# Optimization experiments

Hardware: AMD Instinct MI355X
Metric: run time of the kernel (lower is better)

Reference implementation:

```python
import jax, jax.numpy as jnp
import numpy as np

L = 64      # max source length (x_maxL)
B = 32      # batch
DIN = 512   # input_dim
D = 512     # output_dim
FFS = 512   # filter_feats_size[-1]; conv kernel = 2*D (fwz=2) => Linear(2D -> FFS)


def setup_inputs() -> dict:
    key = jax.random.key(0)
    ks = jax.random.split(key, 5)
    def w(k, shape, fan_in):
        return jax.random.normal(k, shape, jnp.float32) * (1.0 / np.sqrt(fan_in))
    return {
        "xs_h": jax.random.normal(ks[0], (L, B, DIN), jnp.float32),
        "xs_mask": jnp.ones((L, B), jnp.float32),
        "W1": w(ks[1], (D, DIN), DIN),
        "b1": jnp.zeros((D,), jnp.float32),
        "Wc": w(ks[2], (FFS, 2 * D), 2 * D),   # Conv1d weight [FFS,1,2D] squeezed
        "bc": jnp.zeros((FFS,), jnp.float32),
        "W2": w(ks[3], (D, FFS), FFS),
        "b2": jnp.zeros((D,), jnp.float32),
    }


def _cyk_table(xs_h, W1, b1, Wc, bc, W2, b2):
    Lx, Bx, _ = xs_h.shape
    Dd = W1.shape[0]
    # diagonal: table[i][i] = l_f1(xs_h[i])
    diag = xs_h @ W1.T + b1                                  # [L,B,D]
    table = jnp.zeros((Lx, Lx, Bx, Dd), xs_h.dtype)
    ii = jnp.arange(Lx)
    table = table.at[ii, ii].set(diag)
    # wavefront over span length s: all spans (j, j+s) computed together
    for s in range(1, Lx):
        n = Lx - s                    # number of spans of this length
        j = np.arange(n)              # static indices -> efficient gather
        k = np.arange(s)              # split points offset
        left = table[j[:, None], j[:, None] + k[None, :]]            # [n,s,B,D]
        right = table[j[:, None] + k[None, :] + 1, j[:, None] + s]   # [n,s,B,D]
        comb = jnp.concatenate([left, right], axis=-1)               # [n,s,B,2D]
        # Conv1d(1, FFS, kernel=2D, stride=D) on a length-2D signal == Linear(2D->FFS)
        scores = jnp.einsum('nsbd,fd->nsbf', comb, Wc) + bc          # [n,s,B,FFS]
        node = scores.max(axis=1)                                    # max over split k
        vals = node @ W2.T + b2                                      # [n,B,D]
        table = table.at[j, j + s].set(vals)
    return table


def _cyk_mask(xs_mask, Lx):
    tri = jnp.triu(jnp.ones((Lx, Lx), xs_mask.dtype))        # [L,L]
    lengths = xs_mask.sum(axis=0)                            # [B]
    col = jnp.arange(Lx)
    keep = (col[None, :, None] < lengths[None, None, :]).astype(xs_mask.dtype)
    return tri[:, :, None] * keep                            # [L,L,B]


def reference(xs_h, xs_mask, W1, b1, Wc, bc, W2, b2):
    table = _cyk_table(xs_h, W1, b1, Wc, bc, W2, b2)
    cykmask = _cyk_mask(xs_mask, xs_h.shape[0])
    return table, cykmask
```

## Files before the change

kernel.cpp:

```cpp
#include <hip/hip_runtime.h>
#include <hip/hip_fp16.h>


#define Lx 64
#define Bb 32
#define CELLSZ (Bb*512)

typedef __attribute__((ext_vector_type(8))) short short8v;
typedef __attribute__((ext_vector_type(4))) float f32x4;

__device__ __forceinline__ int tri_idx(int a, int c) {
    return a*Lx - (a*(a-1))/2 + (c - a);
}
__device__ __forceinline__ unsigned short f2bf(float x) {
    unsigned u = __float_as_uint(x);
    unsigned r = (u + 0x7FFFu + ((u >> 16) & 1u)) >> 16;
    return (unsigned short)r;
}
__device__ __forceinline__ float bf2f(unsigned short h) {
    return __uint_as_float((unsigned)h << 16);
}
__device__ __forceinline__ size_t frag_i(int r, int c) {
    return (size_t)(r >> 4)*8192 + (c >> 3)*128 + (r & 15)*8 + (c & 7);
}
__device__ __forceinline__ unsigned pk_add_f16(unsigned a, unsigned b) {
    unsigned r;
    asm("v_pk_add_f16 %0, %1, %2" : "=v"(r) : "v"(a), "v"(b));
    return r;
}
__device__ __forceinline__ unsigned pk_max_f16(unsigned a, unsigned b) {
    unsigned r;
    asm("v_pk_max_f16 %0, %1, %2" : "=v"(r) : "v"(a), "v"(b));
    return r;
}
__device__ __forceinline__ float2 h2_to_f2(unsigned u) {
    __half2 h;
    *reinterpret_cast<unsigned*>(&h) = u;
    return __half22float2(h);
}

__device__ __forceinline__ void node_epilogue(
    unsigned a0, unsigned a1, unsigned a2, unsigned a3,
    const float* __restrict__ bc, int f0, int j, int b,
    unsigned short* __restrict__ nodeH, unsigned short* __restrict__ nodeL)
{
    float4 bcA = *(const float4*)(bc + f0);
    float4 bcB = *(const float4*)(bc + f0 + 4);
    float bcv[8] = {bcA.x,bcA.y,bcA.z,bcA.w,bcB.x,bcB.y,bcB.z,bcB.w};
    unsigned am[4] = {a0,a1,a2,a3};
    unsigned uh[4], ul[4];
    #pragma unroll
    for (int e = 0; e < 4; ++e) {
        float2 x = h2_to_f2(am[e]);
        float v0 = x.x + bcv[2*e], v1 = x.y + bcv[2*e+1];
        unsigned short h0 = f2bf(v0), h1 = f2bf(v1);
        unsigned short o0 = f2bf(v0 - bf2f(h0)), o1 = f2bf(v1 - bf2f(h1));
        uh[e] = (unsigned)h0 | ((unsigned)h1 << 16);
        ul[e] = (unsigned)o0 | ((unsigned)o1 << 16);
    }
    size_t fi = (size_t)j*16384 + frag_i(b, f0);
    *(uint4*)(nodeH + fi) = make_uint4(uh[0],uh[1],uh[2],uh[3]);
    *(uint4*)(nodeL + fi) = make_uint4(ul[0],ul[1],ul[2],ul[3]);
}


__global__ void k_zero_lower(float* __restrict__ table) {
    int cell = blockIdx.x >> 4;
    int i = cell >> 6, j = cell & 63;
    if (j >= i) return;
    int sub = blockIdx.x & 15;
    f32x4* p = (f32x4*)(table + (size_t)cell*CELLSZ) + sub*256 + threadIdx.x;
    __builtin_nontemporal_store((f32x4){0.f,0.f,0.f,0.f}, p);
}

__global__ void k_lengths(const float* __restrict__ xs_mask, float* __restrict__ lengths) {
    int b = threadIdx.x;
    if (b < Bb) {
        float s = 0.f;
        for (int i = 0; i < Lx; ++i) s += xs_mask[i*Bb + b];
        lengths[b] = s;
    }
}

__global__ void k_mask(const float* __restrict__ lengths, float* __restrict__ mask_out) {
    int idx = blockIdx.x*256 + threadIdx.x;
    int b = idx & 31;
    int j = (idx >> 5) & 63;
    int i = idx >> 11;
    float v = (j >= i && (float)j < lengths[b]) ? 1.f : 0.f;
    __builtin_nontemporal_store(v, mask_out + idx);
}

__global__ void k_bias(const float* __restrict__ b2, const float* __restrict__ Wc,
                       float* __restrict__ biasBig) {
    int c = blockIdx.x*256 + threadIdx.x;
    if (c >= 1536) return;
    if (c < 512) { biasBig[c] = b2[c]; return; }
    int p = (c - 512) & 511;
    int dofs = (c < 1024) ? 0 : 512;
    float s = 0.f;
    for (int d = 0; d < 512; ++d) s += b2[d] * Wc[p*1024 + dofs + d];
    biasBig[c] = s;
}

__global__ void k_prep_xh(const float* __restrict__ xs_h,
                          unsigned short* __restrict__ xhH, unsigned short* __restrict__ xhL) {
    int gid = blockIdx.x*256 + threadIdx.x;
    int cell = gid >> 14, e = gid & 16383;
    int b = e >> 9, d = e & 511;
    float v = xs_h[gid];
    unsigned short h = f2bf(v);
    size_t fi = (size_t)cell*16384 + frag_i(b, d);
    xhH[fi] = h; xhL[fi] = f2bf(v - bf2f(h));
}

__global__ void k_prep_w1(const float* __restrict__ W1,
                          unsigned short* __restrict__ WH, unsigned short* __restrict__ WL) {
    int gid = blockIdx.x*256 + threadIdx.x;
    int c = gid >> 9, k = gid & 511;
    float v = W1[c*512 + k];
    unsigned short h = f2bf(v);
    size_t fi = frag_i(c, k);
    WH[fi] = h; WL[fi] = f2bf(v - bf2f(h));
}

__global__ void k_prep_b0(const float* __restrict__ Wc,
                          unsigned short* __restrict__ BH, unsigned short* __restrict__ BL) {
    int gid = blockIdx.x*256 + threadIdx.x;
    int c = gid >> 9, k = gid & 511;
    float v = (c < 512) ? Wc[c*1024 + k] : Wc[(c-512)*1024 + 512 + k];
    unsigned short h = f2bf(v);
    size_t fi = frag_i(c, k);
    BH[fi] = h; BL[fi] = f2bf(v - bf2f(h));
}

__global__ void k_gemm_M(const float* __restrict__ W2, const float* __restrict__ Wc,
                         float* __restrict__ BigB) {
    __shared__ float W2s[32][33];
    __shared__ float Wcs[32][33];
    int ftile = blockIdx.x & 15;
    int ptile = blockIdx.x >> 4;
    int f0 = ftile*32, p0 = ptile*32;
    int dofs  = (p0 >= 512) ? 512 : 0;
    int prow0 = (p0 >= 512) ? (p0 - 512) : p0;
    int t = threadIdx.x;
    int ff = t & 31, pg = t >> 5;
    float acc[4] = {0,0,0,0};
    for (int d0 = 0; d0 < 512; d0 += 32) {
        __syncthreads();
        #pragma unroll
        for (int i = 0; i < 4; ++i) {
            int e = t + 256*i;
            int r = e >> 5, cc = e & 31;
            W2s[r][cc] = W2[(d0 + r)*512 + f0 + cc];
            Wcs[r][cc] = Wc[(prow0 + r)*1024 + dofs + d0 + cc];
        }
        __syncthreads();
        #pragma unroll
        for (int dd = 0; dd < 32; ++dd) {
            float w = W2s[dd][ff];
            #pragma unroll
            for (int ii = 0; ii < 4; ++ii)
                acc[ii] += w * Wcs[pg*4 + ii][dd];
        }
    }
    #pragma unroll
    for (int ii = 0; ii < 4; ++ii)
        BigB[(f0 + ff)*1536 + 512 + p0 + pg*4 + ii] = acc[ii];
}

__global__ void k_makeBT(const float* __restrict__ W2, const float* __restrict__ BigB,
                         unsigned short* __restrict__ BTfH, unsigned short* __restrict__ BTfL) {
    int gid = blockIdx.x*256 + threadIdx.x;
    int c = gid >> 9, k = gid & 511;
    float v = (c < 512) ? W2[c*512 + k] : BigB[k*1536 + c];
    unsigned short h = f2bf(v);
    size_t fi = frag_i(c, k);
    BTfH[fi] = h; BTfL[fi] = f2bf(v - bf2f(h));
}

template<int MODE, int NCOLS>
__global__ __launch_bounds__(256) void k_mfma(
    const unsigned short* __restrict__ AH, const unsigned short* __restrict__ AL,
    const unsigned short* __restrict__ BH, const unsigned short* __restrict__ BL,
    const float* __restrict__ bias,
    float* __restrict__ table, __half* __restrict__ P, __half* __restrict__ Q,
    unsigned short* __restrict__ outH, unsigned short* __restrict__ outL)
{
    constexpr int CTILES = NCOLS / 256;
    int cell = blockIdx.x / CTILES;
    int ct   = blockIdx.x % CTILES;
    int t = threadIdx.x;
    int w = t >> 6, l = t & 63;
    int l15 = l & 15, lg = l >> 4;
    int c0 = ct*256 + w*64;

    f32x4 acc[2][4];
    #pragma unroll
    for (int i = 0; i < 2; ++i)
        #pragma unroll
        for (int j = 0; j < 4; ++j) acc[i][j] = (f32x4){0.f,0.f,0.f,0.f};

    size_t lane_off = (size_t)lg*128 + l15*8;
    const unsigned short* aH = AH + (size_t)cell*16384 + lane_off;
    const unsigned short* aL = AL + (size_t)cell*16384 + lane_off;
    const unsigned short* bH = BH + (size_t)(c0 >> 4)*8192 + lane_off;
    const unsigned short* bL = BL + (size_t)(c0 >> 4)*8192 + lane_off;

    #pragma unroll 2
    for (int ks = 0; ks < 16; ++ks) {
        int ko = ks * 512;
        short8v ah0 = *(const short8v*)(aH + ko);
        short8v ah1 = *(const short8v*)(aH + ko + 8192);
        short8v al0 = *(const short8v*)(aL + ko);
        short8v al1 = *(const short8v*)(aL + ko + 8192);
        short8v bh[4], bl[4];
        #pragma unroll
        for (int cf = 0; cf < 4; ++cf) {
            bh[cf] = *(const short8v*)(bH + ko + cf*8192);
            bl[cf] = *(const short8v*)(bL + ko + cf*8192);
        }
        #pragma unroll
        for (int cf = 0; cf < 4; ++cf) {
            acc[0][cf] = __builtin_amdgcn_mfma_f32_16x16x32_bf16(ah0, bh[cf], acc[0][cf], 0, 0, 0);
            acc[1][cf] = __builtin_amdgcn_mfma_f32_16x16x32_bf16(ah1, bh[cf], acc[1][cf], 0, 0, 0);
            acc[0][cf] = __builtin_amdgcn_mfma_f32_16x16x32_bf16(al0, bh[cf], acc[0][cf], 0, 0, 0);
            acc[1][cf] = __builtin_amdgcn_mfma_f32_16x16x32_bf16(al1, bh[cf], acc[1][cf], 0, 0, 0);
            acc[0][cf] = __builtin_amdgcn_mfma_f32_16x16x32_bf16(ah0, bl[cf], acc[0][cf], 0, 0, 0);
            acc[1][cf] = __builtin_amdgcn_mfma_f32_16x16x32_bf16(ah1, bl[cf], acc[1][cf], 0, 0, 0);
        }
    }

    #pragma unroll
    for (int cf = 0; cf < 4; ++cf) {
        int c = c0 + cf*16 + l15;
        if (MODE == 0) {
            float bv = bias[c];
            size_t tbl = (size_t)(cell*65)*CELLSZ;
            #pragma unroll
            for (int rb = 0; rb < 2; ++rb)
                #pragma unroll
                for (int j = 0; j < 4; ++j) {
                    int r = rb*16 + lg*4 + j;
                    float v = acc[rb][cf][j] + bv;
                    __builtin_nontemporal_store(v, table + tbl + (size_t)r*512 + c);
                    size_t fi = (size_t)cell*16384 + frag_i(r, c);
                    unsigned short h = f2bf(v);
                    outH[fi] = h; outL[fi] = f2bf(v - bf2f(h));
                }
        } else {
            int tc = tri_idx(cell, cell);
            __half* dst = (c < 512) ? (P + (size_t)tc*CELLSZ) : (Q + (size_t)tc*CELLSZ);
            int cc = c & 511;
            #pragma unroll
            for (int rb = 0; rb < 2; ++rb)
                #pragma unroll
                for (int j = 0; j < 4; ++j) {
                    int r = rb*16 + lg*4 + j;
                    dst[(size_t)r*512 + cc] = __float2half(acc[rb][cf][j]);
                }
        }
    }
}

__global__ __launch_bounds__(256, 4) void k_node_ml(
    const __half* __restrict__ P, const __half* __restrict__ Q,
    const float* __restrict__ bc,
    unsigned short* __restrict__ nodeH, unsigned short* __restrict__ nodeL,
    __half* __restrict__ nodePart, int s, int KC)
{
    int per_j = KC << 3;
    int j   = blockIdx.x / per_j;
    int rem = blockIdx.x - j*per_j;
    int kc  = rem >> 3, bq = rem & 7;
    int t = threadIdx.x;
    int b  = bq*4 + (t >> 6);
    int f0 = (t & 63) * 8;
    int k0 = (s*kc)/KC, k1 = (s*(kc+1))/KC;

    unsigned A0 = 0xFC00FC00u, A1 = A0, A2 = A0, A3 = A0;
    int basePt = tri_idx(j, j);
    const __half* Pb = P + (size_t)(basePt + k0)*CELLSZ + b*512 + f0;
    const __half* Qb = Q + (size_t)b*512 + f0;
    int aa = j + k0 + 1;
    int tQ = aa*64 - ((aa*(aa-1)) >> 1) + (j + s - aa);
    int k = k0;

    while (k + 8 <= k1) {
        uint4 vp[8], vq[8];
        int tq = tQ, av = aa;
        #pragma unroll
        for (int u = 0; u < 8; ++u) {
            vp[u] = *(const uint4*)(Pb + (size_t)u*CELLSZ);
            vq[u] = *(const uint4*)(Qb + (size_t)tq*CELLSZ);
            tq += 63 - av; ++av;
        }
        #pragma unroll
        for (int u = 0; u < 8; ++u) {
            vp[u].x = pk_add_f16(vp[u].x, vq[u].x);
            vp[u].y = pk_add_f16(vp[u].y, vq[u].y);
            vp[u].z = pk_add_f16(vp[u].z, vq[u].z);
            vp[u].w = pk_add_f16(vp[u].w, vq[u].w);
        }
        #pragma unroll
        for (int st = 4; st >= 1; st >>= 1)
            #pragma unroll
            for (int u = 0; u < st; ++u) {
                vp[u].x = pk_max_f16(vp[u].x, vp[u+st].x);
                vp[u].y = pk_max_f16(vp[u].y, vp[u+st].y);
                vp[u].z = pk_max_f16(vp[u].z, vp[u+st].z);
                vp[u].w = pk_max_f16(vp[u].w, vp[u+st].w);
            }
        A0 = pk_max_f16(A0, vp[0].x);
        A1 = pk_max_f16(A1, vp[0].y);
        A2 = pk_max_f16(A2, vp[0].z);
        A3 = pk_max_f16(A3, vp[0].w);
        tQ = tq; aa = av; k += 8; Pb += (size_t)8*CELLSZ;
    }
    for (; k < k1; ++k) {
        uint4 vp = *(const uint4*)(Pb);
        uint4 vq = *(const uint4*)(Qb + (size_t)tQ*CELLSZ);
        A0 = pk_max_f16(A0, pk_add_f16(vp.x, vq.x));
        A1 = pk_max_f16(A1, pk_add_f16(vp.y, vq.y));
        A2 = pk_max_f16(A2, pk_add_f16(vp.z, vq.z));
        A3 = pk_max_f16(A3, pk_add_f16(vp.w, vq.w));
        tQ += 63 - aa; ++aa; Pb += CELLSZ;
    }

    if (KC == 1) {
        node_epilogue(A0, A1, A2, A3, bc, f0, j, b, nodeH, nodeL);
    } else {
        *(uint4*)(nodePart + (size_t)(kc*32 + j)*CELLSZ + b*512 + f0) =
            make_uint4(A0, A1, A2, A3);
    }
}

__global__ __launch_bounds__(256) void k_node_red(
    const __half* __restrict__ nodePart, const float* __restrict__ bc,
    unsigned short* __restrict__ nodeH, unsigned short* __restrict__ nodeL, int KC)
{
    int j  = blockIdx.x >> 3;
    int bq = blockIdx.x & 7;
    int t = threadIdx.x;
    int b  = bq*4 + (t >> 6);
    int f0 = (t & 63) * 8;
    const __half* base = nodePart + (size_t)j*CELLSZ + b*512 + f0;
    uint4 v = *(const uint4*)(base);
    unsigned A0 = v.x, A1 = v.y, A2 = v.z, A3 = v.w;
    for (int kc = 1; kc < KC; ++kc) {
        uint4 w = *(const uint4*)(base + (size_t)kc*32*CELLSZ);
        A0 = pk_max_f16(A0, w.x);
        A1 = pk_max_f16(A1, w.y);
        A2 = pk_max_f16(A2, w.z);
        A3 = pk_max_f16(A3, w.w);
    }
    node_epilogue(A0, A1, A2, A3, bc, f0, j, b, nodeH, nodeL);
}

__global__ __launch_bounds__(64, 4) void k_gemm_ml(
    const unsigned short* __restrict__ nodeH, const unsigned short* __restrict__ nodeL,
    const unsigned short* __restrict__ BTfH, const unsigned short* __restrict__ BTfL,
    const float* __restrict__ biasBig,
    float* __restrict__ table, __half* __restrict__ P, __half* __restrict__ Q, int s)
{
    int cell = blockIdx.x / 48;
    int tile = blockIdx.x - cell*48;
    int c0   = tile*32;
    int l = threadIdx.x;
    int l15 = l & 15, lg = l >> 4;

    f32x4 acc[2][2];
    #pragma unroll
    for (int i = 0; i < 2; ++i)
        #pragma unroll
        for (int j2 = 0; j2 < 2; ++j2) acc[i][j2] = (f32x4){0.f,0.f,0.f,0.f};

    size_t lane_off = (size_t)lg*128 + l15*8;
    const unsigned short* aH = nodeH + (size_t)cell*16384 + lane_off;
    const unsigned short* aL = nodeL + (size_t)cell*16384 + lane_off;
    const unsigned short* bH = BTfH + (size_t)(c0 >> 4)*8192 + lane_off;
    const unsigned short* bL = BTfL + (size_t)(c0 >> 4)*8192 + lane_off;

    #pragma unroll 4
    for (int ks = 0; ks < 16; ++ks) {
        int ko = ks * 512;
        short8v ah0 = *(const short8v*)(aH + ko);
        short8v ah1 = *(const short8v*)(aH + ko + 8192);
        short8v al0 = *(const short8v*)(aL + ko);
        short8v al1 = *(const short8v*)(aL + ko + 8192);
        short8v bh[2], bl[2];
        #pragma unroll
        for (int cf = 0; cf < 2; ++cf) {
            bh[cf] = *(const short8v*)(bH + ko + cf*8192);
            bl[cf] = *(const short8v*)(bL + ko + cf*8192);
        }
        #pragma unroll
        for (int cf = 0; cf < 2; ++cf) {
            acc[0][cf] = __builtin_amdgcn_mfma_f32_16x16x32_bf16(ah0, bh[cf], acc[0][cf], 0, 0, 0);
            acc[1][cf] = __builtin_amdgcn_mfma_f32_16x16x32_bf16(ah1, bh[cf], acc[1][cf], 0, 0, 0);
            acc[0][cf] = __builtin_amdgcn_mfma_f32_16x16x32_bf16(al0, bh[cf], acc[0][cf], 0, 0, 0);
            acc[1][cf] = __builtin_amdgcn_mfma_f32_16x16x32_bf16(al1, bh[cf], acc[1][cf], 0, 0, 0);
            acc[0][cf] = __builtin_amdgcn_mfma_f32_16x16x32_bf16(ah0, bl[cf], acc[0][cf], 0, 0, 0);
            acc[1][cf] = __builtin_amdgcn_mfma_f32_16x16x32_bf16(ah1, bl[cf], acc[1][cf], 0, 0, 0);
        }
    }

    int tc = tri_idx(cell, cell) + s;
    size_t tbl = (size_t)(cell*64 + cell + s)*CELLSZ;
    #pragma unroll
    for (int cf = 0; cf < 2; ++cf) {
        int c = c0 + cf*16 + l15;
        float bv = biasBig[c];
        #pragma unroll
        for (int rb = 0; rb < 2; ++rb)
            #pragma unroll
            for (int j2 = 0; j2 < 4; ++j2) {
                int r = rb*16 + lg*4 + j2;
                float v = acc[rb][cf][j2] + bv;
                if (c < 512)       __builtin_nontemporal_store(v, table + tbl + (size_t)r*512 + c);
                else if (c < 1024) P[(size_t)tc*CELLSZ + (size_t)r*512 + (c-512)]  = __float2half(v);
                else               Q[(size_t)tc*CELLSZ + (size_t)r*512 + (c-1024)] = __float2half(v);
            }
    }
}


extern "C" void kernel_launch(void* const* d_in, const int* in_sizes, int n_in,
                              void* d_out, int out_size, void* d_ws, size_t ws_size,
                              hipStream_t stream) {
    const float* xs_h    = (const float*)d_in[0];
    const float* xs_mask = (const float*)d_in[1];
    const float* W1      = (const float*)d_in[2];
    const float* b1      = (const float*)d_in[3];
    const float* Wc      = (const float*)d_in[4];
    const float* bc      = (const float*)d_in[5];
    const float* W2      = (const float*)d_in[6];
    const float* b2      = (const float*)d_in[7];

    float* table   = (float*)d_out;
    float* maskout = table + 67108864;

    __half* P = (__half*)d_ws;
    __half* Q = P + 34078720;
    unsigned short* nodeH = (unsigned short*)(Q + 34078720);
    unsigned short* nodeL = nodeH + 1032192;
    unsigned short* xhH   = nodeL + 1032192;
    unsigned short* xhL   = xhH + 1048576;
    unsigned short* diagH = xhL + 1048576;
    unsigned short* diagL = diagH + 1048576;
    unsigned short* W1fH  = diagL + 1048576;
    unsigned short* W1fL  = W1fH + 262144;
    unsigned short* B0fH  = W1fL + 262144;
    unsigned short* B0fL  = B0fH + 524288;
    unsigned short* BTfH  = B0fL + 524288;
    unsigned short* BTfL  = BTfH + 786432;
    float* BigB    = (float*)(BTfL + 786432);
    float* biasBig = BigB + 786432;
    float* lengths = biasBig + 1536;
    __half* nodePart = (__half*)(lengths + 64);

    k_zero_lower<<<65536, 256, 0, stream>>>(table);
    k_lengths<<<1, 64, 0, stream>>>(xs_mask, lengths);
    k_mask<<<512, 256, 0, stream>>>(lengths, maskout);
    k_prep_xh<<<4096, 256, 0, stream>>>(xs_h, xhH, xhL);
    k_prep_w1<<<1024, 256, 0, stream>>>(W1, W1fH, W1fL);
    k_prep_b0<<<2048, 256, 0, stream>>>(Wc, B0fH, B0fL);
    k_gemm_M<<<512, 256, 0, stream>>>(W2, Wc, BigB);
    k_bias<<<6, 256, 0, stream>>>(b2, Wc, biasBig);
    k_makeBT<<<3072, 256, 0, stream>>>(W2, BigB, BTfH, BTfL);

    k_mfma<0, 512><<<64*2, 256, 0, stream>>>(xhH, xhL, W1fH, W1fL, b1,
                                             table, nullptr, nullptr, diagH, diagL);
    k_mfma<1, 1024><<<64*4, 256, 0, stream>>>(diagH, diagL, B0fH, B0fL, nullptr,
                                              table, P, Q, nullptr, nullptr);

    for (int s = 1; s < 64; ++s) {
        int n = 64 - s;
        int KC = (n >= 32) ? 1 : (n >= 16) ? 2 : (n >= 4) ? 4 : 8;
        k_node_ml<<<n*8*KC, 256, 0, stream>>>(P, Q, bc, nodeH, nodeL, nodePart, s, KC);
        if (KC > 1)
            k_node_red<<<n*8, 256, 0, stream>>>(nodePart, bc, nodeH, nodeL, KC);
        k_gemm_ml<<<n*48, 64, 0, stream>>>(nodeH, nodeL, BTfH, BTfL, biasBig,
                                           table, P, Q, s);
    }
}
```

Measured before the change: 1.645 ms.

## Re-layout Q by column and fuse split-K reduction plus GEMM into last block

Stores Q cells in a column-major triangular layout, so the split-point loop reads Q contiguously instead of walking with a variable stride. For spans where the split-K path is used, the separate reduction kernel and the projection GEMM kernel are removed. The last block to finish for each span (detected with an atomic counter) reduces the partials and runs all 48 column tiles of the GEMM itself. This cuts kernel launches for the later wavefront steps, but serialises each cell's GEMM onto a single block of 4 waves and adds an atomic and fence per block.

```diff
diff --git a/kernel.cpp b/kernel.cpp
--- a/kernel.cpp
+++ b/kernel.cpp
@@ -11,6 +11,9 @@
 
 __device__ __forceinline__ int tri_idx(int a, int c) {
     return a*Lx - (a*(a-1))/2 + (c - a);
+}
+__device__ __forceinline__ int qt_idx(int a, int c) {
+    return ((c*(c+1)) >> 1) + a;
 }
 __device__ __forceinline__ unsigned short f2bf(float x) {
     unsigned u = __float_as_uint(x);
@@ -61,6 +64,113 @@
     size_t fi = (size_t)j*16384 + frag_i(b, f0);
     *(uint4*)(nodeH + fi) = make_uint4(uh[0],uh[1],uh[2],uh[3]);
     *(uint4*)(nodeL + fi) = make_uint4(ul[0],ul[1],ul[2],ul[3]);
+}
+
+__device__ __forceinline__ void node_accum2(
+    const __half* __restrict__ Pb, const __half* __restrict__ Qb, int cnt,
+    unsigned &A0, unsigned &A1, unsigned &A2, unsigned &A3)
+{
+    while (cnt >= 8) {
+        uint4 vp[8], vq[8];
+        #pragma unroll
+        for (int u = 0; u < 8; ++u) {
+            vp[u] = *(const uint4*)(Pb + (size_t)u*CELLSZ);
+            vq[u] = *(const uint4*)(Qb + (size_t)u*CELLSZ);
+        }
+        #pragma unroll
+        for (int u = 0; u < 8; ++u) {
+            vp[u].x = pk_add_f16(vp[u].x, vq[u].x);
+            vp[u].y = pk_add_f16(vp[u].y, vq[u].y);
+            vp[u].z = pk_add_f16(vp[u].z, vq[u].z);
+            vp[u].w = pk_add_f16(vp[u].w, vq[u].w);
+        }
+        #pragma unroll
+        for (int st = 4; st >= 1; st >>= 1)
+            #pragma unroll
+            for (int u = 0; u < st; ++u) {
+                vp[u].x = pk_max_f16(vp[u].x, vp[u+st].x);
+                vp[u].y = pk_max_f16(vp[u].y, vp[u+st].y);
+                vp[u].z = pk_max_f16(vp[u].z, vp[u+st].z);
+                vp[u].w = pk_max_f16(vp[u].w, vp[u+st].w);
+            }
+        A0 = pk_max_f16(A0, vp[0].x);
+        A1 = pk_max_f16(A1, vp[0].y);
+        A2 = pk_max_f16(A2, vp[0].z);
+        A3 = pk_max_f16(A3, vp[0].w);
+        Pb += (size_t)8*CELLSZ; Qb += (size_t)8*CELLSZ; cnt -= 8;
+    }
+    for (; cnt > 0; --cnt) {
+        uint4 vp = *(const uint4*)(Pb);
+        uint4 vq = *(const uint4*)(Qb);
+        A0 = pk_max_f16(A0, pk_add_f16(vp.x, vq.x));
+        A1 = pk_max_f16(A1, pk_add_f16(vp.y, vq.y));
+        A2 = pk_max_f16(A2, pk_add_f16(vp.z, vq.z));
+        A3 = pk_max_f16(A3, pk_add_f16(vp.w, vq.w));
+        Pb += CELLSZ; Qb += CELLSZ;
+    }
+}
+
+__device__ __forceinline__ void gemm_tile32(
+    int cell, int c0, int s, int l15, int lg,
+    const unsigned short* __restrict__ nodeH, const unsigned short* __restrict__ nodeL,
+    const unsigned short* __restrict__ BTfH, const unsigned short* __restrict__ BTfL,
+    const float* __restrict__ biasBig,
+    float* __restrict__ table, __half* __restrict__ P, __half* __restrict__ Qt)
+{
+    f32x4 acc[2][2];
+    #pragma unroll
+    for (int i = 0; i < 2; ++i)
+        #pragma unroll
+        for (int j2 = 0; j2 < 2; ++j2) acc[i][j2] = (f32x4){0.f,0.f,0.f,0.f};
+
+    size_t lane_off = (size_t)lg*128 + l15*8;
+    const unsigned short* aH = nodeH + (size_t)cell*16384 + lane_off;
+    const unsigned short* aL = nodeL + (size_t)cell*16384 + lane_off;
+    const unsigned short* bH = BTfH + (size_t)(c0 >> 4)*8192 + lane_off;
+    const unsigned short* bL = BTfL + (size_t)(c0 >> 4)*8192 + lane_off;
+
+    #pragma unroll 4
+    for (int ks = 0; ks < 16; ++ks) {
+        int ko = ks * 512;
+        short8v ah0 = *(const short8v*)(aH + ko);
+        short8v ah1 = *(const short8v*)(aH + ko + 8192);
+        short8v al0 = *(const short8v*)(aL + ko);
+        short8v al1 = *(const short8v*)(aL + ko + 8192);
+        short8v bh[2], bl[2];
+        #pragma unroll
+        for (int cf = 0; cf < 2; ++cf) {
+            bh[cf] = *(const short8v*)(bH + ko + cf*8192);
+            bl[cf] = *(const short8v*)(bL + ko + cf*8192);
+        }
+        #pragma unroll
+        for (int cf = 0; cf < 2; ++cf) {
+            acc[0][cf] = __builtin_amdgcn_mfma_f32_16x16x32_bf16(ah0, bh[cf], acc[0][cf], 0, 0, 0);
+            acc[1][cf] = __builtin_amdgcn_mfma_f32_16x16x32_bf16(ah1, bh[cf], acc[1][cf], 0, 0, 0);
+            acc[0][cf] = __builtin_amdgcn_mfma_f32_16x16x32_bf16(al0, bh[cf], acc[0][cf], 0, 0, 0);
+            acc[1][cf] = __builtin_amdgcn_mfma_f32_16x16x32_bf16(al1, bh[cf], acc[1][cf], 0, 0, 0);
+            acc[0][cf] = __builtin_amdgcn_mfma_f32_16x16x32_bf16(ah0, bl[cf], acc[0][cf], 0, 0, 0);
+            acc[1][cf] = __builtin_amdgcn_mfma_f32_16x16x32_bf16(ah1, bl[cf], acc[1][cf], 0, 0, 0);
+        }
+    }
+
+    int tcP = tri_idx(cell, cell) + s;
+    int tcQ = qt_idx(cell, cell + s);
+    size_t tbl = (size_t)(cell*64 + cell + s)*CELLSZ;
+    #pragma unroll
+    for (int cf = 0; cf < 2; ++cf) {
+        int c = c0 + cf*16 + l15;
+        float bv = biasBig[c];
+        #pragma unroll
+        for (int rb = 0; rb < 2; ++rb)
+            #pragma unroll
+            for (int j2 = 0; j2 < 4; ++j2) {
+                int r = rb*16 + lg*4 + j2;
+                float v = acc[rb][cf][j2] + bv;
+                if (c < 512)       __builtin_nontemporal_store(v, table + tbl + (size_t)r*512 + c);
+                else if (c < 1024) P[(size_t)tcP*CELLSZ + (size_t)r*512 + (c-512)]  = __float2half(v);
+                else               Qt[(size_t)tcQ*CELLSZ + (size_t)r*512 + (c-1024)] = __float2half(v);
+            }
+    }
 }
 
 
@@ -184,7 +294,7 @@
     const unsigned short* __restrict__ AH, const unsigned short* __restrict__ AL,
     const unsigned short* __restrict__ BH, const unsigned short* __restrict__ BL,
     const float* __restrict__ bias,
-    float* __restrict__ table, __half* __restrict__ P, __half* __restrict__ Q,
+    float* __restrict__ table, __half* __restrict__ P, __half* __restrict__ Qt,
     unsigned short* __restrict__ outH, unsigned short* __restrict__ outL)
 {
     constexpr int CTILES = NCOLS / 256;
@@ -249,8 +359,9 @@
                     outH[fi] = h; outL[fi] = f2bf(v - bf2f(h));
                 }
         } else {
-            int tc = tri_idx(cell, cell);
-            __half* dst = (c < 512) ? (P + (size_t)tc*CELLSZ) : (Q + (size_t)tc*CELLSZ);
+            int tcP = tri_idx(cell, cell);
+            int tcQ = qt_idx(cell, cell);
+            __half* dst = (c < 512) ? (P + (size_t)tcP*CELLSZ) : (Qt + (size_t)tcQ*CELLSZ);
             int cc = c & 511;
             #pragma unroll
             for (int rb = 0; rb < 2; ++rb)
@@ -264,10 +375,14 @@
 }
 
 __global__ __launch_bounds__(256, 4) void k_node_ml(
-    const __half* __restrict__ P, const __half* __restrict__ Q,
+    const __half* __restrict__ P, const __half* __restrict__ Qt,
     const float* __restrict__ bc,
     unsigned short* __restrict__ nodeH, unsigned short* __restrict__ nodeL,
-    __half* __restrict__ nodePart, int s, int KC)
+    __half* __restrict__ nodePart,
+    const unsigned short* __restrict__ BTfH, const unsigned short* __restrict__ BTfL,
+    const float* __restrict__ biasBig,
+    float* __restrict__ table, __half* __restrict__ Pw, __half* __restrict__ Qtw,
+    int* __restrict__ done, int s, int KC)
 {
     int per_j = KC << 3;
     int j   = blockIdx.x / per_j;
@@ -279,149 +394,69 @@
     int k0 = (s*kc)/KC, k1 = (s*(kc+1))/KC;
 
     unsigned A0 = 0xFC00FC00u, A1 = A0, A2 = A0, A3 = A0;
-    int basePt = tri_idx(j, j);
-    const __half* Pb = P + (size_t)(basePt + k0)*CELLSZ + b*512 + f0;
-    const __half* Qb = Q + (size_t)b*512 + f0;
-    int aa = j + k0 + 1;
-    int tQ = aa*64 - ((aa*(aa-1)) >> 1) + (j + s - aa);
-    int k = k0;
-
-    while (k + 8 <= k1) {
-        uint4 vp[8], vq[8];
-        int tq = tQ, av = aa;
-        #pragma unroll
-        for (int u = 0; u < 8; ++u) {
-            vp[u] = *(const uint4*)(Pb + (size_t)u*CELLSZ);
-            vq[u] = *(const uint4*)(Qb + (size_t)tq*CELLSZ);
-            tq += 63 - av; ++av;
-        }
-        #pragma unroll
-        for (int u = 0; u < 8; ++u) {
-            vp[u].x = pk_add_f16(vp[u].x, vq[u].x);
-            vp[u].y = pk_add_f16(vp[u].y, vq[u].y);
-            vp[u].z = pk_add_f16(vp[u].z, vq[u].z);
-            vp[u].w = pk_add_f16(vp[u].w, vq[u].w);
-        }
-        #pragma unroll
-        for (int st = 4; st >= 1; st >>= 1)
-            #pragma unroll
-            for (int u = 0; u < st; ++u) {
-                vp[u].x = pk_max_f16(vp[u].x, vp[u+st].x);
-                vp[u].y = pk_max_f16(vp[u].y, vp[u+st].y);
-                vp[u].z = pk_max_f16(vp[u].z, vp[u+st].z);
-                vp[u].w = pk_max_f16(vp[u].w, vp[u+st].w);
-            }
-        A0 = pk_max_f16(A0, vp[0].x);
-        A1 = pk_max_f16(A1, vp[0].y);
-        A2 = pk_max_f16(A2, vp[0].z);
-        A3 = pk_max_f16(A3, vp[0].w);
-        tQ = tq; aa = av; k += 8; Pb += (size_t)8*CELLSZ;
-    }
-    for (; k < k1; ++k) {
-        uint4 vp = *(const uint4*)(Pb);
-        uint4 vq = *(const uint4*)(Qb + (size_t)tQ*CELLSZ);
-        A0 = pk_max_f16(A0, pk_add_f16(vp.x, vq.x));
-        A1 = pk_max_f16(A1, pk_add_f16(vp.y, vq.y));
-        A2 = pk_max_f16(A2, pk_add_f16(vp.z, vq.z));
-        A3 = pk_max_f16(A3, pk_add_f16(vp.w, vq.w));
-        tQ += 63 - aa; ++aa; Pb += CELLSZ;
-    }
+    int C = j + s;
+    const __half* Pb = P  + (size_t)(tri_idx(j, j) + k0)*CELLSZ + b*512 + f0;
+    const __half* Qb = Qt + (size_t)(qt_idx(j + 1, C) + k0)*CELLSZ + b*512 + f0;
+    node_accum2(Pb, Qb, k1 - k0, A0, A1, A2, A3);
 
     if (KC == 1) {
         node_epilogue(A0, A1, A2, A3, bc, f0, j, b, nodeH, nodeL);
-    } else {
-        *(uint4*)(nodePart + (size_t)(kc*32 + j)*CELLSZ + b*512 + f0) =
-            make_uint4(A0, A1, A2, A3);
-    }
-}
-
-__global__ __launch_bounds__(256) void k_node_red(
-    const __half* __restrict__ nodePart, const float* __restrict__ bc,
-    unsigned short* __restrict__ nodeH, unsigned short* __restrict__ nodeL, int KC)
-{
-    int j  = blockIdx.x >> 3;
-    int bq = blockIdx.x & 7;
-    int t = threadIdx.x;
-    int b  = bq*4 + (t >> 6);
-    int f0 = (t & 63) * 8;
-    const __half* base = nodePart + (size_t)j*CELLSZ + b*512 + f0;
-    uint4 v = *(const uint4*)(base);
-    unsigned A0 = v.x, A1 = v.y, A2 = v.z, A3 = v.w;
-    for (int kc = 1; kc < KC; ++kc) {
-        uint4 w = *(const uint4*)(base + (size_t)kc*32*CELLSZ);
-        A0 = pk_max_f16(A0, w.x);
-        A1 = pk_max_f16(A1, w.y);
-        A2 = pk_max_f16(A2, w.z);
-        A3 = pk_max_f16(A3, w.w);
-    }
-    node_epilogue(A0, A1, A2, A3, bc, f0, j, b, nodeH, nodeL);
+        return;
+    }
+
+    *(uint4*)(nodePart + (size_t)(kc*32 + j)*CELLSZ + b*512 + f0) =
+        make_uint4(A0, A1, A2, A3);
+
+    __shared__ int lastFlag;
+    __syncthreads();
+    if (t == 0) {
+        int old = __hip_atomic_fetch_add(&done[(s << 6) + j], 1,
+                                         __ATOMIC_RELEASE, __HIP_MEMORY_SCOPE_AGENT);
+        lastFlag = (old == (KC << 3) - 1);
+        if (lastFlag) __builtin_amdgcn_fence(__ATOMIC_ACQUIRE, "agent");
+    }
+    __syncthreads();
+    if (!lastFlag) return;
+
+    int bw = t >> 6;
+    #pragma unroll
+    for (int bb = 0; bb < 8; ++bb) {
+        int b2 = bw + 4*bb;
+        const __half* base = nodePart + (size_t)j*CELLSZ + b2*512 + f0;
+        uint4 v = *(const uint4*)(base);
+        unsigned R0 = v.x, R1 = v.y, R2 = v.z, R3 = v.w;
+        for (int c2 = 1; c2 < KC; ++c2) {
+            uint4 w2 = *(const uint4*)(base + (size_t)c2*32*CELLSZ);
+            R0 = pk_max_f16(R0, w2.x);
+            R1 = pk_max_f16(R1, w2.y);
+            R2 = pk_max_f16(R2, w2.z);
+            R3 = pk_max_f16(R3, w2.w);
+        }
+        node_epilogue(R0, R1, R2, R3, bc, f0, j, b2, nodeH, nodeL);
+    }
+    __syncthreads();
+
+    int l = t & 63;
+    int l15 = l & 15, lg = l >> 4;
+    int w = t >> 6;
+    for (int tt = 0; tt < 12; ++tt) {
+        int c0 = (tt*4 + w) * 32;
+        gemm_tile32(j, c0, s, l15, lg, nodeH, nodeL, BTfH, BTfL, biasBig,
+                    table, Pw, Qtw);
+    }
 }
 
 __global__ __launch_bounds__(64, 4) void k_gemm_ml(
     const unsigned short* __restrict__ nodeH, const unsigned short* __restrict__ nodeL,
     const unsigned short* __restrict__ BTfH, const unsigned short* __restrict__ BTfL,
     const float* __restrict__ biasBig,
-    float* __restrict__ table, __half* __restrict__ P, __half* __restrict__ Q, int s)
+    float* __restrict__ table, __half* __restrict__ P, __half* __restrict__ Qt, int s)
 {
     int cell = blockIdx.x / 48;
     int tile = blockIdx.x - cell*48;
-    int c0   = tile*32;
     int l = threadIdx.x;
-    int l15 = l & 15, lg = l >> 4;
-
-    f32x4 acc[2][2];
-    #pragma unroll
-    for (int i = 0; i < 2; ++i)
-        #pragma unroll
-        for (int j2 = 0; j2 < 2; ++j2) acc[i][j2] = (f32x4){0.f,0.f,0.f,0.f};
-
-    size_t lane_off = (size_t)lg*128 + l15*8;
-    const unsigned short* aH = nodeH + (size_t)cell*16384 + lane_off;
-    const unsigned short* aL = nodeL + (size_t)cell*16384 + lane_off;
-    const unsigned short* bH = BTfH + (size_t)(c0 >> 4)*8192 + lane_off;
-    const unsigned short* bL = BTfL + (size_t)(c0 >> 4)*8192 + lane_off;
-
-    #pragma unroll 4
-    for (int ks = 0; ks < 16; ++ks) {
-        int ko = ks * 512;
-        short8v ah0 = *(const short8v*)(aH + ko);
-        short8v ah1 = *(const short8v*)(aH + ko + 8192);
-        short8v al0 = *(const short8v*)(aL + ko);
-        short8v al1 = *(const short8v*)(aL + ko + 8192);
-        short8v bh[2], bl[2];
-        #pragma unroll
-        for (int cf = 0; cf < 2; ++cf) {
-            bh[cf] = *(const short8v*)(bH + ko + cf*8192);
-            bl[cf] = *(const short8v*)(bL + ko + cf*8192);
-        }
-        #pragma unroll
-        for (int cf = 0; cf < 2; ++cf) {
-            acc[0][cf] = __builtin_amdgcn_mfma_f32_16x16x32_bf16(ah0, bh[cf], acc[0][cf], 0, 0, 0);
-            acc[1][cf] = __builtin_amdgcn_mfma_f32_16x16x32_bf16(ah1, bh[cf], acc[1][cf], 0, 0, 0);
-            acc[0][cf] = __builtin_amdgcn_mfma_f32_16x16x32_bf16(al0, bh[cf], acc[0][cf], 0, 0, 0);
-            acc[1][cf] = __builtin_amdgcn_mfma_f32_16x16x32_bf16(al1, bh[cf], acc[1][cf], 0, 0, 0);
-            acc[0][cf] = __builtin_amdgcn_mfma_f32_16x16x32_bf16(ah0, bl[cf], acc[0][cf], 0, 0, 0);
-            acc[1][cf] = __builtin_amdgcn_mfma_f32_16x16x32_bf16(ah1, bl[cf], acc[1][cf], 0, 0, 0);
-        }
-    }
-
-    int tc = tri_idx(cell, cell) + s;
-    size_t tbl = (size_t)(cell*64 + cell + s)*CELLSZ;
-    #pragma unroll
-    for (int cf = 0; cf < 2; ++cf) {
-        int c = c0 + cf*16 + l15;
-        float bv = biasBig[c];
-        #pragma unroll
-        for (int rb = 0; rb < 2; ++rb)
-            #pragma unroll
-            for (int j2 = 0; j2 < 4; ++j2) {
-                int r = rb*16 + lg*4 + j2;
-                float v = acc[rb][cf][j2] + bv;
-                if (c < 512)       __builtin_nontemporal_store(v, table + tbl + (size_t)r*512 + c);
-                else if (c < 1024) P[(size_t)tc*CELLSZ + (size_t)r*512 + (c-512)]  = __float2half(v);
-                else               Q[(size_t)tc*CELLSZ + (size_t)r*512 + (c-1024)] = __float2half(v);
-            }
-    }
+    gemm_tile32(cell, tile*32, s, l & 15, l >> 4, nodeH, nodeL, BTfH, BTfL, biasBig,
+                table, P, Qt);
 }
 
 
@@ -440,9 +475,9 @@
     float* table   = (float*)d_out;
     float* maskout = table + 67108864;
 
-    __half* P = (__half*)d_ws;
-    __half* Q = P + 34078720;
-    unsigned short* nodeH = (unsigned short*)(Q + 34078720);
+    __half* P  = (__half*)d_ws;
+    __half* Qt = P + 34078720;
+    unsigned short* nodeH = (unsigned short*)(Qt + 34078720);
     unsigned short* nodeL = nodeH + 1032192;
     unsigned short* xhH   = nodeL + 1032192;
     unsigned short* xhL   = xhH + 1048576;
@@ -457,8 +492,10 @@
     float* BigB    = (float*)(BTfL + 786432);
     float* biasBig = BigB + 786432;
     float* lengths = biasBig + 1536;
-    __half* nodePart = (__half*)(lengths + 64);
-
+    int*   done    = (int*)(lengths + 64);
+    __half* nodePart = (__half*)(done + 4096);
+
+    (void)hipMemsetAsync(done, 0, 4096*4, stream);
     k_zero_lower<<<65536, 256, 0, stream>>>(table);
     k_lengths<<<1, 64, 0, stream>>>(xs_mask, lengths);
     k_mask<<<512, 256, 0, stream>>>(lengths, maskout);
@@ -472,15 +509,16 @@
     k_mfma<0, 512><<<64*2, 256, 0, stream>>>(xhH, xhL, W1fH, W1fL, b1,
                                              table, nullptr, nullptr, diagH, diagL);
     k_mfma<1, 1024><<<64*4, 256, 0, stream>>>(diagH, diagL, B0fH, B0fL, nullptr,
-                                              table, P, Q, nullptr, nullptr);
+                                              table, P, Qt, nullptr, nullptr);
 
     for (int s = 1; s < 64; ++s) {
         int n = 64 - s;
         int KC = (n >= 32) ? 1 : (n >= 16) ? 2 : (n >= 4) ? 4 : 8;
-        k_node_ml<<<n*8*KC, 256, 0, stream>>>(P, Q, bc, nodeH, nodeL, nodePart, s, KC);
-        if (KC > 1)
-            k_node_red<<<n*8, 256, 0, stream>>>(nodePart, bc, nodeH, nodeL, KC);
-        k_gemm_ml<<<n*48, 64, 0, stream>>>(nodeH, nodeL, BTfH, BTfL, biasBig,
-                                           table, P, Q, s);
-    }
-}
+        k_node_ml<<<n*8*KC, 256, 0, stream>>>(P, Qt, bc, nodeH, nodeL, nodePart,
+                                              BTfH, BTfL, biasBig, table, P, Qt,
+                                              done, s, KC);
+        if (KC == 1)
+            k_gemm_ml<<<n*48, 64, 0, stream>>>(nodeH, nodeL, BTfH, BTfL, biasBig,
+                                               table, P, Qt, s);
+    }
+}
```

Result: slower. 5.016 ms (+205.0%).
